# Kernel optimization log

Measured on AMD Instinct MI355X. Metric: run time of the kernel, lower is better.

The kernel has to match this reference:

```python
import jax, jax.numpy as jnp
import numpy as np

S, NPS = 64, 48           # scenes, agents per scene
H, A = 256, 64            # edge_hidden_size, attention_dim
N = S * NPS


def setup_inputs() -> dict:
    key = jax.random.key(0)
    ks = jax.random.split(key, 6)
    spatial_ht = jax.random.normal(ks[0], (S, NPS, NPS, H), dtype=jnp.float32)
    temporal_ht = jax.random.normal(ks[1], (N, H), dtype=jnp.float32)
    ts_mask = jax.random.randint(ks[2], (N, 1), 0, 2).astype(jnp.int32)
    same_scene_mask = jnp.repeat(jnp.arange(S, dtype=jnp.int32), NPS)[:, None]
    # small init keeps exp(score) in-range (original uses raw, unstabilized exp)
    W1_w = jax.random.normal(ks[3], (A, H), dtype=jnp.float32) * 0.02
    W1_b = jnp.zeros((A,), dtype=jnp.float32)
    W2_w = jax.random.normal(ks[4], (A, H), dtype=jnp.float32) * 0.02
    W2_b = jnp.zeros((A,), dtype=jnp.float32)
    return {"spatial_ht": spatial_ht, "temporal_ht": temporal_ht,
            "W1_w": W1_w, "W1_b": W1_b, "W2_w": W2_w, "W2_b": W2_b,
            "ts_mask": ts_mask, "same_scene_mask": same_scene_mask}


def reference(spatial_ht, temporal_ht, W1_w, W1_b, W2_w, W2_b, ts_mask, same_scene_mask):
    # spatial_ht: [S, n, n, H] (stacked per-scene blocks), temporal_ht: [S*n, H]
    S_, n = spatial_ht.shape[0], spatial_ht.shape[1]
    Hd = spatial_ht.shape[-1]
    A_ = W1_w.shape[0]
    dt = spatial_ht.dtype

    m = (ts_mask[:, 0] == 1).reshape(S_, n)            # [S, n] existence mask
    ne = jnp.sum(m, axis=1).astype(dt)                  # [S] existing agents per scene

    # W1(spatial edge states), W2(temporal state of row agent i, broadcast over j)
    proj_s = jnp.einsum('snjh,ah->snja', spatial_ht, W1_w) + W1_b      # [S,n,n,A]
    t = temporal_ht.reshape(S_, n, Hd)
    proj_t = jnp.einsum('snh,ah->sna', t, W2_w) + W2_b                 # [S,n,A]

    score = jnp.einsum('snja,sna->snj', proj_s, proj_t)                # [S,n,n]
    score = score * ne[:, None, None] / jnp.sqrt(jnp.asarray(A_, dt))

    eye = jnp.eye(n, dtype=bool)
    valid = m[:, :, None] & m[:, None, :] & ~eye[None]                 # off-diag, both exist
    num = jnp.where(valid, jnp.exp(jnp.where(valid, score, 0.0)), 0.0)
    den = jnp.sum(num, axis=2, keepdims=True)                          # [S,n,1]
    attn = num / jnp.where(den > 0, den, 1.0)                          # zeros for absent rows / ne<=1 scenes

    # edge-to-node aggregation: sum_j attn[i,j] * spatial_ht[i,j,:]
    out = jnp.einsum('snjh,snj->snh', spatial_ht, attn)                # [S,n,H]
    return out.reshape(S_ * n, Hd)
```

## Files before the change

### kernel.cpp

```cpp
#include <hip/hip_runtime.h>

#define Hd 256
#define NPSd 48
#define Sd 64
#define Nd (Sd*NPSd)
#define ROWS 4

__device__ __forceinline__ void barrier_lds() {
  asm volatile("s_waitcnt lgkmcnt(0)" ::: "memory");
  __builtin_amdgcn_s_barrier();
}

__global__ __launch_bounds__(256) void fused_kernel(
    const float* __restrict__ spatial,
    const float* __restrict__ temporal,
    const float* __restrict__ W1_w, const float* __restrict__ W1_b,
    const float* __restrict__ W2_w, const float* __restrict__ W2_b,
    const int* __restrict__ ts_mask,
    float* __restrict__ out) {
  __shared__ float t_lds[ROWS][4][72];
  __shared__ float pt_lds[ROWS][64];
  __shared__ float crp[4][ROWS];
  __shared__ float vred[ROWS][4][Hd];
  __shared__ float vvL[ROWS][Hd];
  __shared__ float crL[ROWS];

  int row0 = blockIdx.x * ROWS;
  int s    = row0 / NPSd;
  int i0   = row0 - s*NPSd;
  int tid  = threadIdx.x;
  int wave = tid >> 6, lane = tid & 63;

  int al = (wave<<4) + (lane & 15);
  int q  = lane >> 4;
  float b1v = W1_b[al];
  float b2v = W2_b[al];

  {
    int r = tid >> 6, h4 = (tid & 63) << 2;
    float4 tv = *(const float4*)(temporal + (size_t)(row0 + r)*Hd + h4);
    *(float4*)&t_lds[r][h4 >> 6][h4 & 63] = tv;
  }

  float4 w2r[16];
#pragma unroll
  for (int m = 0; m < 16; ++m)
    w2r[m] = *(const float4*)(W2_w + (size_t)al*Hd + q*64 + m*4);

  __syncthreads();

#pragma unroll
  for (int r = 0; r < ROWS; ++r) {
    float p = 0.f;
#pragma unroll
    for (int m = 0; m < 16; ++m) {
      float4 wv = w2r[m];
      p += wv.x * t_lds[r][q][m*4+0];
      p += wv.y * t_lds[r][q][m*4+1];
      p += wv.z * t_lds[r][q][m*4+2];
      p += wv.w * t_lds[r][q][m*4+3];
    }
    p += __shfl_xor(p, 16);
    p += __shfl_xor(p, 32);
    float pfull = p + b2v;
    float cb = pfull * b1v;
    cb += __shfl_xor(cb, 1);
    cb += __shfl_xor(cb, 2);
    cb += __shfl_xor(cb, 4);
    cb += __shfl_xor(cb, 8);
    if (lane < 16) pt_lds[r][(wave<<4) + lane] = pfull;
    if (lane == 0) crp[wave][r] = cb;
  }
  barrier_lds();

  float4 w1r[16];
#pragma unroll
  for (int j = 0; j < 16; ++j)
    w1r[j] = *(const float4*)(W1_w + (size_t)((wave<<4)+j)*Hd + (lane<<2));

#pragma unroll
  for (int r = 0; r < ROWS; ++r) {
    float4 v4 = make_float4(0.f,0.f,0.f,0.f);
#pragma unroll
    for (int j = 0; j < 16; ++j) {
      float pj = pt_lds[r][(wave<<4)+j];
      float4 wv = w1r[j];
      v4.x += pj*wv.x; v4.y += pj*wv.y; v4.z += pj*wv.z; v4.w += pj*wv.w;
    }
    *(float4*)&vred[r][wave][lane<<2] = v4;
  }
  barrier_lds();

#pragma unroll
  for (int r = 0; r < ROWS; ++r)
    vvL[r][tid] = vred[r][0][tid] + vred[r][1][tid]
                + vred[r][2][tid] + vred[r][3][tid];
  if (tid < ROWS)
    crL[tid] = crp[0][tid] + crp[1][tid] + crp[2][tid] + crp[3][tid];
  barrier_lds();

  int row  = row0 + wave;
  int irow = i0 + wave;

  int ml = lane < NPSd ? lane : NPSd-1;
  int mv = ts_mask[s*NPSd + ml];
  unsigned long long mb = __ballot(mv == 1 && lane < NPSd);
  int nv = __popcll(mb);
  float scale = (float)nv * 0.125f;
  bool rowv = (mb >> (unsigned)irow) & 1ULL;

  float4 vv = *(const float4*)&vvL[wave][lane<<2];
  float cr = crL[wave];

  float4 o4 = make_float4(0.f, 0.f, 0.f, 0.f);
  float den = 0.f;

  if (rowv && nv > 1) {
    unsigned long long m = mb;
    int k = lane, jbit = 0, pc;
    pc = __popcll(m & 0xFFFFFFFFull); if (k >= pc) { jbit += 32; k -= pc; m >>= 32; }
    pc = __popcll(m & 0xFFFFull);     if (k >= pc) { jbit += 16; k -= pc; m >>= 16; }
    pc = __popcll(m & 0xFFull);       if (k >= pc) { jbit += 8;  k -= pc; m >>= 8; }
    pc = __popcll(m & 0xFull);        if (k >= pc) { jbit += 4;  k -= pc; m >>= 4; }
    pc = __popcll(m & 0x3ull);        if (k >= pc) { jbit += 2;  k -= pc; m >>= 2; }
    pc = (int)(m & 1ull);             if (k >= pc) { jbit += 1; }

    const float* rb = spatial + (size_t)row*NPSd*Hd;
    int nc = (nv + 3) >> 2;
    float4 A[4], B[4], C[4];
    int jA[4], jB[4], jC[4];

#define ISSUE(DST, JD, Ch)                                                  \
    { _Pragma("unroll")                                                     \
      for (int rr = 0; rr < 4; ++rr) {                                      \
        int slot = (Ch)*4 + rr;                                             \
        int ss = slot < nv ? slot : 0;                                      \
        int j = __shfl(jbit, ss);                                           \
        JD[rr] = slot < nv ? j : -1;                                        \
        DST[rr] = *(const float4*)(rb + (size_t)j*Hd + (lane << 2));        \
      }                                                                     \
      __builtin_amdgcn_sched_barrier(0); }

#define DO_CHUNK(CUR, JC2)                                                  \
    { _Pragma("unroll")                                                     \
      for (int rr = 0; rr < 4; ++rr) {                                      \
        int j = JC2[rr];                                                    \
        float4 a4 = CUR[rr];                                                \
        float pp = a4.x*vv.x + a4.y*vv.y + a4.z*vv.z + a4.w*vv.w;           \
        pp += __shfl_xor(pp, 1);                                            \
        pp += __shfl_xor(pp, 2);                                            \
        pp += __shfl_xor(pp, 4);                                            \
        pp += __shfl_xor(pp, 8);                                            \
        pp += __shfl_xor(pp, 16);                                           \
        pp += __shfl_xor(pp, 32);                                           \
        bool valid = (j >= 0) && (j != irow);                               \
        float nj = valid ? __expf((pp + cr) * scale) : 0.f;                 \
        den += nj;                                                          \
        o4.x += nj*a4.x; o4.y += nj*a4.y; o4.z += nj*a4.z; o4.w += nj*a4.w; \
      } }

    ISSUE(A, jA, 0);
    if (nc > 1) ISSUE(B, jB, 1);
    if (nc > 2) ISSUE(C, jC, 2);
    int cc = 0;
    while (true) {
      DO_CHUNK(A, jA); if (cc + 3 < nc) ISSUE(A, jA, cc + 3);
      ++cc; if (cc >= nc) break;
      DO_CHUNK(B, jB); if (cc + 3 < nc) ISSUE(B, jB, cc + 3);
      ++cc; if (cc >= nc) break;
      DO_CHUNK(C, jC); if (cc + 3 < nc) ISSUE(C, jC, cc + 3);
      ++cc; if (cc >= nc) break;
    }
#undef ISSUE
#undef DO_CHUNK
  }

  float inv = den > 0.f ? 1.f/den : 0.f;
  o4.x *= inv; o4.y *= inv; o4.z *= inv; o4.w *= inv;
  *(float4*)(out + (size_t)row*Hd + (lane<<2)) = o4;
}

extern "C" void kernel_launch(void* const* d_in, const int* in_sizes, int n_in,
                              void* d_out, int out_size, void* d_ws, size_t ws_size,
                              hipStream_t stream) {
  const float* spatial  = (const float*)d_in[0];
  const float* temporal = (const float*)d_in[1];
  const float* W1_w     = (const float*)d_in[2];
  const float* W1_b     = (const float*)d_in[3];
  const float* W2_w     = (const float*)d_in[4];
  const float* W2_b     = (const float*)d_in[5];
  const int*   ts_mask  = (const int*)d_in[6];
  float* out = (float*)d_out;

  fused_kernel<<<Nd/ROWS, 256, 0, stream>>>(spatial, temporal, W1_w, W1_b,
                                            W2_w, W2_b, ts_mask, out);
}
```

Baseline: 23.99 us.

## Split neighbor rows across waves, prefetch spatial rows, early-exit empty blocks

Instead of each wave handling one output row, all four waves of a block now share the neighbor loads for every valid row in the block: each wave takes every fourth neighbor slot. Partial sums and denominators are then reduced through LDS before normalising. The first chunk of spatial loads is issued before the W1 projection and LDS reductions, so global-memory latency overlaps with that compute. Blocks whose rows are all absent, or whose scene has at most one agent, write zeros and return right away. The costs are an extra LDS reduction pass, a barrier, and more live registers for the prefetched data.

```diff
diff --git a/kernel.cpp b/kernel.cpp
--- a/kernel.cpp
+++ b/kernel.cpp
@@ -24,6 +24,7 @@
   __shared__ float vred[ROWS][4][Hd];
   __shared__ float vvL[ROWS][Hd];
   __shared__ float crL[ROWS];
+  __shared__ float denr[ROWS][4];
 
   int row0 = blockIdx.x * ROWS;
   int s    = row0 / NPSd;
@@ -31,6 +32,34 @@
   int tid  = threadIdx.x;
   int wave = tid >> 6, lane = tid & 63;
 
+  int ml = lane < NPSd ? lane : NPSd-1;
+  int mv = ts_mask[s*NPSd + ml];
+  unsigned long long mb = __ballot(mv == 1 && lane < NPSd);
+  int nv = __popcll(mb);
+  unsigned rbits = (unsigned)((mb >> (unsigned)i0) & 0xFull);
+  if (nv <= 1 || rbits == 0u) {
+    float4 z = make_float4(0.f,0.f,0.f,0.f);
+    *(float4*)(out + (size_t)(row0 + wave)*Hd + (lane<<2)) = z;
+    return;
+  }
+  float scale = (float)nv * 0.125f;
+
+  {
+  }
+  unsigned long long m = mb;
+  int k = lane, jbit = 0, pc;
+  pc = __popcll(m & 0xFFFFFFFFull); if (k >= pc) { jbit += 32; k -= pc; m >>= 32; }
+  pc = __popcll(m & 0xFFFFull);     if (k >= pc) { jbit += 16; k -= pc; m >>= 16; }
+  pc = __popcll(m & 0xFFull);       if (k >= pc) { jbit += 8;  k -= pc; m >>= 8; }
+  pc = __popcll(m & 0xFull);        if (k >= pc) { jbit += 4;  k -= pc; m >>= 4; }
+  pc = __popcll(m & 0x3ull);        if (k >= pc) { jbit += 2;  k -= pc; m >>= 2; }
+  pc = (int)(m & 1ull);             if (k >= pc) { jbit += 1; }
+
+  unsigned vrpack = 0; int nvr = 0;
+#pragma unroll
+  for (int r = 0; r < 4; ++r)
+    if ((rbits >> r) & 1u) { vrpack |= (unsigned)r << (8*nvr); ++nvr; }
+
   int al = (wave<<4) + (lane & 15);
   int q  = lane >> 4;
   float b1v = W1_b[al];
@@ -44,8 +73,8 @@
 
   float4 w2r[16];
 #pragma unroll
-  for (int m = 0; m < 16; ++m)
-    w2r[m] = *(const float4*)(W2_w + (size_t)al*Hd + q*64 + m*4);
+  for (int mm = 0; mm < 16; ++mm)
+    w2r[mm] = *(const float4*)(W2_w + (size_t)al*Hd + q*64 + mm*4);
 
   __syncthreads();
 
@@ -53,12 +82,12 @@
   for (int r = 0; r < ROWS; ++r) {
     float p = 0.f;
 #pragma unroll
-    for (int m = 0; m < 16; ++m) {
-      float4 wv = w2r[m];
-      p += wv.x * t_lds[r][q][m*4+0];
-      p += wv.y * t_lds[r][q][m*4+1];
-      p += wv.z * t_lds[r][q][m*4+2];
-      p += wv.w * t_lds[r][q][m*4+3];
+    for (int mm = 0; mm < 16; ++mm) {
+      float4 wv = w2r[mm];
+      p += wv.x * t_lds[r][q][mm*4+0];
+      p += wv.y * t_lds[r][q][mm*4+1];
+      p += wv.z * t_lds[r][q][mm*4+2];
+      p += wv.w * t_lds[r][q][mm*4+3];
     }
     p += __shfl_xor(p, 16);
     p += __shfl_xor(p, 32);
@@ -77,6 +106,43 @@
 #pragma unroll
   for (int j = 0; j < 16; ++j)
     w1r[j] = *(const float4*)(W1_w + (size_t)((wave<<4)+j)*Hd + (lane<<2));
+  __builtin_amdgcn_sched_barrier(0);
+
+#define ISSUE(DST, JD, RL, CH)                                              \
+  { const float* rbm = spatial + (size_t)(row0 + (RL))*NPSd*Hd;             \
+    _Pragma("unroll")                                                       \
+    for (int rr = 0; rr < 4; ++rr) {                                        \
+      int slot = wave + 4*((CH)*4 + rr);                                    \
+      bool sval = slot < nv;                                                \
+      int ss = sval ? slot : 0;                                             \
+      int j = __shfl(jbit, ss);                                             \
+      JD[rr] = sval ? j : -1;                                               \
+      DST[rr] = *(const float4*)(rbm + (size_t)j*Hd + (lane << 2));         \
+    }                                                                       \
+    __builtin_amdgcn_sched_barrier(0); }
+
+#define DO_CHUNK(CUR, JC2, IROW, VV, CR)                                    \
+  { _Pragma("unroll")                                                       \
+    for (int rr = 0; rr < 4; ++rr) {                                        \
+      int j = JC2[rr];                                                      \
+      float4 a4 = CUR[rr];                                                  \
+      float pp = a4.x*(VV).x + a4.y*(VV).y + a4.z*(VV).z + a4.w*(VV).w;     \
+      pp += __shfl_xor(pp, 1);                                              \
+      pp += __shfl_xor(pp, 2);                                              \
+      pp += __shfl_xor(pp, 4);                                              \
+      pp += __shfl_xor(pp, 8);                                              \
+      pp += __shfl_xor(pp, 16);                                             \
+      pp += __shfl_xor(pp, 32);                                             \
+      bool valid = (j >= 0) && (j != (IROW));                               \
+      float nj = valid ? __expf((pp + (CR)) * scale) : 0.f;                 \
+      den += nj;                                                            \
+      o4.x += nj*a4.x; o4.y += nj*a4.y; o4.z += nj*a4.z; o4.w += nj*a4.w;   \
+    } }
+
+  float4 A[4], B[4], C[4];
+  int jA[4], jB[4], jC[4];
+  int r0v = (int)(vrpack & 0xFFu);
+  ISSUE(A, jA, r0v, 0);
 
 #pragma unroll
   for (int r = 0; r < ROWS; ++r) {
@@ -99,85 +165,54 @@
     crL[tid] = crp[0][tid] + crp[1][tid] + crp[2][tid] + crp[3][tid];
   barrier_lds();
 
-  int row  = row0 + wave;
-  int irow = i0 + wave;
-
-  int ml = lane < NPSd ? lane : NPSd-1;
-  int mv = ts_mask[s*NPSd + ml];
-  unsigned long long mb = __ballot(mv == 1 && lane < NPSd);
-  int nv = __popcll(mb);
-  float scale = (float)nv * 0.125f;
-  bool rowv = (mb >> (unsigned)irow) & 1ULL;
-
-  float4 vv = *(const float4*)&vvL[wave][lane<<2];
-  float cr = crL[wave];
-
-  float4 o4 = make_float4(0.f, 0.f, 0.f, 0.f);
-  float den = 0.f;
-
-  if (rowv && nv > 1) {
-    unsigned long long m = mb;
-    int k = lane, jbit = 0, pc;
-    pc = __popcll(m & 0xFFFFFFFFull); if (k >= pc) { jbit += 32; k -= pc; m >>= 32; }
-    pc = __popcll(m & 0xFFFFull);     if (k >= pc) { jbit += 16; k -= pc; m >>= 16; }
-    pc = __popcll(m & 0xFFull);       if (k >= pc) { jbit += 8;  k -= pc; m >>= 8; }
-    pc = __popcll(m & 0xFull);        if (k >= pc) { jbit += 4;  k -= pc; m >>= 4; }
-    pc = __popcll(m & 0x3ull);        if (k >= pc) { jbit += 2;  k -= pc; m >>= 2; }
-    pc = (int)(m & 1ull);             if (k >= pc) { jbit += 1; }
-
-    const float* rb = spatial + (size_t)row*NPSd*Hd;
-    int nc = (nv + 3) >> 2;
-    float4 A[4], B[4], C[4];
-    int jA[4], jB[4], jC[4];
-
-#define ISSUE(DST, JD, Ch)                                                  \
-    { _Pragma("unroll")                                                     \
-      for (int rr = 0; rr < 4; ++rr) {                                      \
-        int slot = (Ch)*4 + rr;                                             \
-        int ss = slot < nv ? slot : 0;                                      \
-        int j = __shfl(jbit, ss);                                           \
-        JD[rr] = slot < nv ? j : -1;                                        \
-        DST[rr] = *(const float4*)(rb + (size_t)j*Hd + (lane << 2));        \
-      }                                                                     \
-      __builtin_amdgcn_sched_barrier(0); }
-
-#define DO_CHUNK(CUR, JC2)                                                  \
-    { _Pragma("unroll")                                                     \
-      for (int rr = 0; rr < 4; ++rr) {                                      \
-        int j = JC2[rr];                                                    \
-        float4 a4 = CUR[rr];                                                \
-        float pp = a4.x*vv.x + a4.y*vv.y + a4.z*vv.z + a4.w*vv.w;           \
-        pp += __shfl_xor(pp, 1);                                            \
-        pp += __shfl_xor(pp, 2);                                            \
-        pp += __shfl_xor(pp, 4);                                            \
-        pp += __shfl_xor(pp, 8);                                            \
-        pp += __shfl_xor(pp, 16);                                           \
-        pp += __shfl_xor(pp, 32);                                           \
-        bool valid = (j >= 0) && (j != irow);                               \
-        float nj = valid ? __expf((pp + cr) * scale) : 0.f;                 \
-        den += nj;                                                          \
-        o4.x += nj*a4.x; o4.y += nj*a4.y; o4.z += nj*a4.z; o4.w += nj*a4.w; \
-      } }
-
-    ISSUE(A, jA, 0);
-    if (nc > 1) ISSUE(B, jB, 1);
-    if (nc > 2) ISSUE(C, jC, 2);
-    int cc = 0;
-    while (true) {
-      DO_CHUNK(A, jA); if (cc + 3 < nc) ISSUE(A, jA, cc + 3);
-      ++cc; if (cc >= nc) break;
-      DO_CHUNK(B, jB); if (cc + 3 < nc) ISSUE(B, jB, cc + 3);
-      ++cc; if (cc >= nc) break;
-      DO_CHUNK(C, jC); if (cc + 3 < nc) ISSUE(C, jC, cc + 3);
-      ++cc; if (cc >= nc) break;
-    }
+  for (int ri = 0; ri < nvr; ++ri) {
+    int r = (int)((vrpack >> (8*ri)) & 0xFFu);
+    int irowr = i0 + r;
+    float4 vv = *(const float4*)&vvL[r][lane<<2];
+    float cr = crL[r];
+    float4 o4 = make_float4(0.f,0.f,0.f,0.f);
+    float den = 0.f;
+
+    if (4 + wave < nv)  ISSUE(B, jB, r, 1);
+    if (32 + wave < nv) ISSUE(C, jC, r, 2);
+    DO_CHUNK(A, jA, irowr, vv, cr);
+    if (ri + 1 < nvr) {
+      int rn = (int)((vrpack >> (8*(ri+1))) & 0xFFu);
+      ISSUE(A, jA, rn, 0);
+    }
+    if (4 + wave < nv) { DO_CHUNK(B, jB, irowr, vv, cr); }
+    else {
+#pragma unroll
+      for (int rr = 0; rr < 4; ++rr) jB[rr] = -1;
+    }
+    if (32 + wave < nv) { DO_CHUNK(C, jC, irowr, vv, cr); }
+
+    *(float4*)&vred[r][wave][lane<<2] = o4;
+    if (lane == 0) denr[r][wave] = den;
+  }
+  barrier_lds();
+
 #undef ISSUE
 #undef DO_CHUNK
-  }
-
-  float inv = den > 0.f ? 1.f/den : 0.f;
-  o4.x *= inv; o4.y *= inv; o4.z *= inv; o4.w *= inv;
-  *(float4*)(out + (size_t)row*Hd + (lane<<2)) = o4;
+
+  {
+    int r = wave;
+    if ((rbits >> r) & 1u) {
+      float dt = denr[r][0] + denr[r][1] + denr[r][2] + denr[r][3];
+      float4 o = make_float4(0.f,0.f,0.f,0.f);
+#pragma unroll
+      for (int wv = 0; wv < 4; ++wv) {
+        float4 t4 = *(const float4*)&vred[r][wv][lane<<2];
+        o.x += t4.x; o.y += t4.y; o.z += t4.z; o.w += t4.w;
+      }
+      float inv = dt > 0.f ? 1.f/dt : 0.f;
+      o.x *= inv; o.y *= inv; o.z *= inv; o.w *= inv;
+      *(float4*)(out + (size_t)(row0 + r)*Hd + (lane<<2)) = o;
+    } else {
+      float4 z = make_float4(0.f,0.f,0.f,0.f);
+      *(float4*)(out + (size_t)(row0 + r)*Hd + (lane<<2)) = z;
+    }
+  }
 }
 
 extern "C" void kernel_launch(void* const* d_in, const int* in_sizes, int n_in,
```

New measurement: 24.75 us. 1.03x slower.

## Prefetch first spatial chunk early and use DPP wave reductions

Applied to the files above, without the earlier changes.

Moves the mask ballot and valid-index computation to the start of the kernel so the first chunk of spatial rows can be loaded before the W1 projection and LDS reductions, overlapping that global latency with the prologue. The per-edge 64-lane dot-product reduction switches from six shuffle-xor steps to DPP row shifts plus four readlanes. Index broadcasts use readlane instead of shuffle. This raises register pressure, since A[] stays live across the prologue, in exchange for hiding memory latency and cutting LDS-based shuffle traffic.

```diff
diff --git a/kernel.cpp b/kernel.cpp
--- a/kernel.cpp
+++ b/kernel.cpp
@@ -9,6 +9,24 @@
 __device__ __forceinline__ void barrier_lds() {
   asm volatile("s_waitcnt lgkmcnt(0)" ::: "memory");
   __builtin_amdgcn_s_barrier();
+}
+
+__device__ __forceinline__ float wave_sum64(float x) {
+  float v = x;
+  int t;
+  t = __builtin_amdgcn_update_dpp(0, __float_as_int(v), 0x121, 0xF, 0xF, true);
+  v += __int_as_float(t);
+  t = __builtin_amdgcn_update_dpp(0, __float_as_int(v), 0x122, 0xF, 0xF, true);
+  v += __int_as_float(t);
+  t = __builtin_amdgcn_update_dpp(0, __float_as_int(v), 0x124, 0xF, 0xF, true);
+  v += __int_as_float(t);
+  t = __builtin_amdgcn_update_dpp(0, __float_as_int(v), 0x128, 0xF, 0xF, true);
+  v += __int_as_float(t);
+  float g0 = __int_as_float(__builtin_amdgcn_readlane(__float_as_int(v), 0));
+  float g1 = __int_as_float(__builtin_amdgcn_readlane(__float_as_int(v), 16));
+  float g2 = __int_as_float(__builtin_amdgcn_readlane(__float_as_int(v), 32));
+  float g3 = __int_as_float(__builtin_amdgcn_readlane(__float_as_int(v), 48));
+  return (g0 + g1) + (g2 + g3);
 }
 
 __global__ __launch_bounds__(256) void fused_kernel(
@@ -31,6 +49,24 @@
   int tid  = threadIdx.x;
   int wave = tid >> 6, lane = tid & 63;
 
+  int ml = lane < NPSd ? lane : NPSd-1;
+  int mv = ts_mask[s*NPSd + ml];
+  unsigned long long mb = __ballot(mv == 1 && lane < NPSd);
+  int nv = __popcll(mb);
+  float scale = (float)nv * 0.125f;
+  int row  = row0 + wave;
+  int irow = i0 + wave;
+  bool rowv = ((mb >> (unsigned)irow) & 1ULL) && nv > 1;
+
+  unsigned long long m = mb;
+  int k = lane, jbit = 0, pc;
+  pc = __popcll(m & 0xFFFFFFFFull); if (k >= pc) { jbit += 32; k -= pc; m >>= 32; }
+  pc = __popcll(m & 0xFFFFull);     if (k >= pc) { jbit += 16; k -= pc; m >>= 16; }
+  pc = __popcll(m & 0xFFull);       if (k >= pc) { jbit += 8;  k -= pc; m >>= 8; }
+  pc = __popcll(m & 0xFull);        if (k >= pc) { jbit += 4;  k -= pc; m >>= 4; }
+  pc = __popcll(m & 0x3ull);        if (k >= pc) { jbit += 2;  k -= pc; m >>= 2; }
+  pc = (int)(m & 1ull);             if (k >= pc) { jbit += 1; }
+
   int al = (wave<<4) + (lane & 15);
   int q  = lane >> 4;
   float b1v = W1_b[al];
@@ -44,8 +80,8 @@
 
   float4 w2r[16];
 #pragma unroll
-  for (int m = 0; m < 16; ++m)
-    w2r[m] = *(const float4*)(W2_w + (size_t)al*Hd + q*64 + m*4);
+  for (int mm = 0; mm < 16; ++mm)
+    w2r[mm] = *(const float4*)(W2_w + (size_t)al*Hd + q*64 + mm*4);
 
   __syncthreads();
 
@@ -53,12 +89,12 @@
   for (int r = 0; r < ROWS; ++r) {
     float p = 0.f;
 #pragma unroll
-    for (int m = 0; m < 16; ++m) {
-      float4 wv = w2r[m];
-      p += wv.x * t_lds[r][q][m*4+0];
-      p += wv.y * t_lds[r][q][m*4+1];
-      p += wv.z * t_lds[r][q][m*4+2];
-      p += wv.w * t_lds[r][q][m*4+3];
+    for (int mm = 0; mm < 16; ++mm) {
+      float4 wv = w2r[mm];
+      p += wv.x * t_lds[r][q][mm*4+0];
+      p += wv.y * t_lds[r][q][mm*4+1];
+      p += wv.z * t_lds[r][q][mm*4+2];
+      p += wv.w * t_lds[r][q][mm*4+3];
     }
     p += __shfl_xor(p, 16);
     p += __shfl_xor(p, 32);
@@ -77,6 +113,25 @@
 #pragma unroll
   for (int j = 0; j < 16; ++j)
     w1r[j] = *(const float4*)(W1_w + (size_t)((wave<<4)+j)*Hd + (lane<<2));
+  __builtin_amdgcn_sched_barrier(0);
+
+  const float* rb = spatial + (size_t)row*NPSd*Hd;
+  int nc = (nv + 3) >> 2;
+  float4 A[4], B[4], C[4];
+  int jA[4], jB[4], jC[4];
+
+#define ISSUE(DST, JD, Ch)                                                  \
+  { _Pragma("unroll")                                                       \
+    for (int rr = 0; rr < 4; ++rr) {                                        \
+      int slot = (Ch)*4 + rr;                                               \
+      int ss = slot < nv ? slot : 0;                                        \
+      int j = __builtin_amdgcn_readlane(jbit, ss);                          \
+      JD[rr] = slot < nv ? j : -1;                                          \
+      DST[rr] = *(const float4*)(rb + (size_t)j*Hd + (lane << 2));          \
+    }                                                                       \
+    __builtin_amdgcn_sched_barrier(0); }
+
+  if (rowv) { ISSUE(A, jA, 0); }
 
 #pragma unroll
   for (int r = 0; r < ROWS; ++r) {
@@ -99,67 +154,25 @@
     crL[tid] = crp[0][tid] + crp[1][tid] + crp[2][tid] + crp[3][tid];
   barrier_lds();
 
-  int row  = row0 + wave;
-  int irow = i0 + wave;
-
-  int ml = lane < NPSd ? lane : NPSd-1;
-  int mv = ts_mask[s*NPSd + ml];
-  unsigned long long mb = __ballot(mv == 1 && lane < NPSd);
-  int nv = __popcll(mb);
-  float scale = (float)nv * 0.125f;
-  bool rowv = (mb >> (unsigned)irow) & 1ULL;
-
   float4 vv = *(const float4*)&vvL[wave][lane<<2];
   float cr = crL[wave];
-
   float4 o4 = make_float4(0.f, 0.f, 0.f, 0.f);
   float den = 0.f;
 
-  if (rowv && nv > 1) {
-    unsigned long long m = mb;
-    int k = lane, jbit = 0, pc;
-    pc = __popcll(m & 0xFFFFFFFFull); if (k >= pc) { jbit += 32; k -= pc; m >>= 32; }
-    pc = __popcll(m & 0xFFFFull);     if (k >= pc) { jbit += 16; k -= pc; m >>= 16; }
-    pc = __popcll(m & 0xFFull);       if (k >= pc) { jbit += 8;  k -= pc; m >>= 8; }
-    pc = __popcll(m & 0xFull);        if (k >= pc) { jbit += 4;  k -= pc; m >>= 4; }
-    pc = __popcll(m & 0x3ull);        if (k >= pc) { jbit += 2;  k -= pc; m >>= 2; }
-    pc = (int)(m & 1ull);             if (k >= pc) { jbit += 1; }
-
-    const float* rb = spatial + (size_t)row*NPSd*Hd;
-    int nc = (nv + 3) >> 2;
-    float4 A[4], B[4], C[4];
-    int jA[4], jB[4], jC[4];
-
-#define ISSUE(DST, JD, Ch)                                                  \
-    { _Pragma("unroll")                                                     \
-      for (int rr = 0; rr < 4; ++rr) {                                      \
-        int slot = (Ch)*4 + rr;                                             \
-        int ss = slot < nv ? slot : 0;                                      \
-        int j = __shfl(jbit, ss);                                           \
-        JD[rr] = slot < nv ? j : -1;                                        \
-        DST[rr] = *(const float4*)(rb + (size_t)j*Hd + (lane << 2));        \
-      }                                                                     \
-      __builtin_amdgcn_sched_barrier(0); }
-
 #define DO_CHUNK(CUR, JC2)                                                  \
-    { _Pragma("unroll")                                                     \
-      for (int rr = 0; rr < 4; ++rr) {                                      \
-        int j = JC2[rr];                                                    \
-        float4 a4 = CUR[rr];                                                \
-        float pp = a4.x*vv.x + a4.y*vv.y + a4.z*vv.z + a4.w*vv.w;           \
-        pp += __shfl_xor(pp, 1);                                            \
-        pp += __shfl_xor(pp, 2);                                            \
-        pp += __shfl_xor(pp, 4);                                            \
-        pp += __shfl_xor(pp, 8);                                            \
-        pp += __shfl_xor(pp, 16);                                           \
-        pp += __shfl_xor(pp, 32);                                           \
-        bool valid = (j >= 0) && (j != irow);                               \
-        float nj = valid ? __expf((pp + cr) * scale) : 0.f;                 \
-        den += nj;                                                          \
-        o4.x += nj*a4.x; o4.y += nj*a4.y; o4.z += nj*a4.z; o4.w += nj*a4.w; \
-      } }
-
-    ISSUE(A, jA, 0);
+  { _Pragma("unroll")                                                       \
+    for (int rr = 0; rr < 4; ++rr) {                                        \
+      int j = JC2[rr];                                                      \
+      float4 a4 = CUR[rr];                                                  \
+      float pp = a4.x*vv.x + a4.y*vv.y + a4.z*vv.z + a4.w*vv.w;             \
+      float tot = wave_sum64(pp);                                           \
+      bool valid = (j >= 0) && (j != irow);                                 \
+      float nj = valid ? __expf((tot + cr) * scale) : 0.f;                  \
+      den += nj;                                                            \
+      o4.x += nj*a4.x; o4.y += nj*a4.y; o4.z += nj*a4.z; o4.w += nj*a4.w;   \
+    } }
+
+  if (rowv) {
     if (nc > 1) ISSUE(B, jB, 1);
     if (nc > 2) ISSUE(C, jC, 2);
     int cc = 0;
@@ -171,9 +184,9 @@
       DO_CHUNK(C, jC); if (cc + 3 < nc) ISSUE(C, jC, cc + 3);
       ++cc; if (cc >= nc) break;
     }
+  }
 #undef ISSUE
 #undef DO_CHUNK
-  }
 
   float inv = den > 0.f ? 1.f/den : 0.f;
   o4.x *= inv; o4.y *= inv; o4.z *= inv; o4.w *= inv;
```

Result: faster. 22.09 us (-7.9%).
